# Performance work log

Hardware: AMD Instinct MI355X
Metric: run time of the kernel (lower is better)

## Reference

```python
import jax, jax.numpy as jnp
import numpy as np

NUM_RAYS = 262144   # 512x512 image
NUM_BINS = 128      # coarse samples per ray
NUM_SAMPLES = 128   # fine samples per ray (init arg)
EPS = 1e-05


def setup_inputs() -> dict:
    key = jax.random.key(0)
    k1, k2 = jax.random.split(key)
    weights = jax.random.uniform(k1, (NUM_RAYS, NUM_BINS), dtype=jnp.float32)
    u = jax.random.uniform(k2, (NUM_RAYS, NUM_SAMPLES), dtype=jnp.float32)
    return {"weights": weights, "u": u, "stratified": 1}


def reference(weights, u, stratified):
    # --- pdf normalization (visible torch code) ---
    num_bins = weights.shape[-1]
    num_samples = u.shape[-1]
    weights_sum = jnp.sum(weights, axis=-1, keepdims=True)
    padding = jax.nn.relu(EPS - weights_sum)
    weights = weights + padding / num_bins
    weights_sum = weights_sum + padding
    pdf = weights / weights_sum                                   # [R, B]

    # --- CDF ---
    cdf = jnp.cumsum(pdf, axis=-1)
    cdf = jnp.concatenate([jnp.zeros_like(cdf[..., :1]), cdf], axis=-1)  # [R, B+1]

    # --- stratified / deterministic uniforms in [0,1) ---
    strata = jnp.arange(num_samples, dtype=weights.dtype)
    if stratified:
        us = (strata + u) / num_samples                           # [R, S]
    else:
        us = jnp.broadcast_to((strata + 0.5) / num_samples, u.shape)

    # --- inverse-CDF: searchsorted + gather + lerp ---
    inds = jax.vmap(lambda c, uu: jnp.searchsorted(c, uu, side='right'))(cdf, us)
    below = jnp.clip(inds - 1, 0, num_bins)                       # [R, S]
    above = jnp.clip(inds, 0, num_bins)
    cdf_b = jnp.take_along_axis(cdf, below, axis=-1)
    cdf_a = jnp.take_along_axis(cdf, above, axis=-1)
    bins = jnp.linspace(0.0, 1.0, num_bins + 1, dtype=weights.dtype)  # normalized bin edges
    bins_b = bins[below]
    bins_a = bins[above]
    denom = cdf_a - cdf_b
    denom = jnp.where(denom < 1e-5, jnp.ones_like(denom), denom)
    t = (us - cdf_b) / denom
    samples = bins_b + t * (bins_a - bins_b)                      # [R, S]
    return samples
```

## Files before the change

### kernel.cpp

```cpp
#include <hip/hip_runtime.h>


typedef float f32x4 __attribute__((ext_vector_type(4)));

constexpr int NUM_BINS = 128;
constexpr float EPS_PAD = 1e-5f;
constexpr float INV_S   = 1.0f / 128.0f;
constexpr int RPB       = 8;

template <int CTRL, int ROW_MASK>
__device__ __forceinline__ float dpp_add(float x) {
    int s = __builtin_amdgcn_update_dpp(0, __float_as_int(x), CTRL, ROW_MASK, 0xf, true);
    return x + __int_as_float(s);
}

__global__ __launch_bounds__(256) void ray_sampler_kernel(
    const float* __restrict__ W,
    const float* __restrict__ U,
    const int*   __restrict__ stratp,
    float*       __restrict__ out)
{
    const int wave = threadIdx.x >> 6;
    const int lane = threadIdx.x & 63;
    const int h    = lane >> 5;
    const int sl   = lane & 31;
    const int ray  = blockIdx.x * RPB + wave * 2 + h;

    __shared__ float cdf_s[RPB][NUM_BINS];
    float* cw = cdf_s[wave * 2 + h];

    const size_t rb = (size_t)ray * NUM_BINS;
    const int strat = *stratp;

    const float ur0 = U[rb + sl];
    const float ur1 = U[rb + sl + 32];
    const float ur2 = U[rb + sl + 64];
    const float ur3 = U[rb + sl + 96];

    const int b = 4 * sl;
    const f32x4 w4 = *reinterpret_cast<const f32x4*>(W + rb + b);

    const float s1 = w4.x;
    const float s2 = s1 + w4.y;
    const float s3 = s2 + w4.z;
    const float quad = s3 + w4.w;

    float incl = quad;
    incl = dpp_add<0x111, 0xf>(incl);
    incl = dpp_add<0x112, 0xf>(incl);
    incl = dpp_add<0x114, 0xf>(incl);
    incl = dpp_add<0x118, 0xf>(incl);
    incl = dpp_add<0x142, 0xa>(incl);

    const float tot = __shfl(incl, 31 | (lane & 32), 64);
    const float padding = fmaxf(EPS_PAD - tot, 0.0f);
    const float ppb     = padding * INV_S;
    const float inv     = __builtin_amdgcn_rcpf(tot + padding);
    const float pre     = incl - quad;

    f32x4 st;
    st.x = (pre + s1   + (float)(b + 1) * ppb) * inv;
    st.y = (pre + s2   + (float)(b + 2) * ppb) * inv;
    st.z = (pre + s3   + (float)(b + 3) * ppb) * inv;
    st.w = (pre + quad + (float)(b + 4) * ppb) * inv;
    *reinterpret_cast<f32x4*>(cw + b) = st;

    asm volatile("s_waitcnt lgkmcnt(0)" ::: "memory");

    const float uu0 = strat ? ur0 : 0.5f;
    const float uu1 = strat ? ur1 : 0.5f;
    const float uu2 = strat ? ur2 : 0.5f;
    const float uu3 = strat ? ur3 : 0.5f;
    const float us0 = ((float)(sl)      + uu0) * INV_S;
    const float us1 = ((float)(sl + 32) + uu1) * INV_S;
    const float us2 = ((float)(sl + 64) + uu2) * INV_S;
    const float us3 = ((float)(sl + 96) + uu3) * INV_S;

    int a0 = 0, a1 = 0, a2 = 0, a3 = 0;
    #pragma unroll
    for (int step = 64; step; step >>= 1) {
        const float c0 = cw[a0 + (step - 1)];
        const float c1 = cw[a1 + (step - 1)];
        const float c2 = cw[a2 + (step - 1)];
        const float c3 = cw[a3 + (step - 1)];
        if (c0 <= us0) a0 += step;
        if (c1 <= us1) a1 += step;
        if (c2 <= us2) a2 += step;
        if (c3 <= us3) a3 += step;
    }

    const int m0 = a0 ? a0 - 1 : 0;
    const int m1 = a1 ? a1 - 1 : 0;
    const int m2 = a2 ? a2 - 1 : 0;
    const int m3 = a3 ? a3 - 1 : 0;
    const float lo0 = cw[m0], hi0 = cw[m0 + 1];
    const float lo1 = cw[m1], hi1 = cw[m1 + 1];
    const float lo2 = cw[m2], hi2 = cw[m2 + 1];
    const float lo3 = cw[m3], hi3 = cw[m3 + 1];
    const float cb0 = a0 ? lo0 : 0.0f, ca0 = a0 ? hi0 : lo0;
    const float cb1 = a1 ? lo1 : 0.0f, ca1 = a1 ? hi1 : lo1;
    const float cb2 = a2 ? lo2 : 0.0f, ca2 = a2 ? hi2 : lo2;
    const float cb3 = a3 ? lo3 : 0.0f, ca3 = a3 ? hi3 : lo3;

    float d0 = ca0 - cb0;  d0 = (d0 < 1e-5f) ? 1.0f : d0;
    float d1 = ca1 - cb1;  d1 = (d1 < 1e-5f) ? 1.0f : d1;
    float d2 = ca2 - cb2;  d2 = (d2 < 1e-5f) ? 1.0f : d2;
    float d3 = ca3 - cb3;  d3 = (d3 < 1e-5f) ? 1.0f : d3;

    const float o0 = ((float)a0 + (us0 - cb0) * __builtin_amdgcn_rcpf(d0)) * INV_S;
    const float o1 = ((float)a1 + (us1 - cb1) * __builtin_amdgcn_rcpf(d1)) * INV_S;
    const float o2 = ((float)a2 + (us2 - cb2) * __builtin_amdgcn_rcpf(d2)) * INV_S;
    const float o3 = ((float)a3 + (us3 - cb3) * __builtin_amdgcn_rcpf(d3)) * INV_S;

    __builtin_nontemporal_store(o0, out + rb + sl);
    __builtin_nontemporal_store(o1, out + rb + sl + 32);
    __builtin_nontemporal_store(o2, out + rb + sl + 64);
    __builtin_nontemporal_store(o3, out + rb + sl + 96);
}

extern "C" void kernel_launch(void* const* d_in, const int* in_sizes, int n_in,
                              void* d_out, int out_size, void* d_ws, size_t ws_size,
                              hipStream_t stream) {
    const float* W     = (const float*)d_in[0];
    const float* U     = (const float*)d_in[1];
    const int*   strat = (const int*)d_in[2];
    float*       out   = (float*)d_out;

    const int num_rays = in_sizes[0] / NUM_BINS;
    const int blocks   = num_rays / RPB;
    hipLaunchKernelGGL(ray_sampler_kernel, dim3(blocks), dim3(256), 0, stream,
                       W, U, strat, out);
}
```

Baseline: 60.57 us.

## Resolve top binary-search levels from registers and use bit-reversed LDS layout

The CDF is now stored in LDS in a bit-reversed (Eytzinger-like) order, and the first three binary-search levels take their pivots from readlane'd scalar values instead of LDS. The remaining four levels read LDS at addresses that fit the bit-reversed layout, and the lower/upper CDF bracket is tracked during the search, so the final two gathers go away. The shuffle for the row total is replaced with readlanes. This cuts LDS traffic and dependent LDS latency on the search path, at the cost of scalar readlanes, extra selects, and scalar LDS stores in place of a vector store.

```diff
diff --git a/kernel.cpp b/kernel.cpp
--- a/kernel.cpp
+++ b/kernel.cpp
@@ -12,6 +12,10 @@
 __device__ __forceinline__ float dpp_add(float x) {
     int s = __builtin_amdgcn_update_dpp(0, __float_as_int(x), CTRL, ROW_MASK, 0xf, true);
     return x + __int_as_float(s);
+}
+
+__device__ __forceinline__ float rl(float v, int lane) {
+    return __int_as_float(__builtin_amdgcn_readlane(__float_as_int(v), lane));
 }
 
 __global__ __launch_bounds__(256) void ray_sampler_kernel(
@@ -39,7 +43,6 @@
 
     const int b = 4 * sl;
     const f32x4 w4 = *reinterpret_cast<const f32x4*>(W + rb + b);
-
     const float s1 = w4.x;
     const float s2 = s1 + w4.y;
     const float s3 = s2 + w4.z;
@@ -52,7 +55,8 @@
     incl = dpp_add<0x118, 0xf>(incl);
     incl = dpp_add<0x142, 0xa>(incl);
 
-    const float tot = __shfl(incl, 31 | (lane & 32), 64);
+    const float totA = rl(incl, 31), totB = rl(incl, 63);
+    const float tot  = h ? totB : totA;
     const float padding = fmaxf(EPS_PAD - tot, 0.0f);
     const float ppb     = padding * INV_S;
     const float inv     = __builtin_amdgcn_rcpf(tot + padding);
@@ -63,7 +67,21 @@
     st.y = (pre + s2   + (float)(b + 2) * ppb) * inv;
     st.z = (pre + s3   + (float)(b + 3) * ppb) * inv;
     st.w = (pre + quad + (float)(b + 4) * ppb) * inv;
-    *reinterpret_cast<f32x4*>(cw + b) = st;
+
+    const int r5 = (int)(__brev((unsigned)sl) >> 27);
+    cw[r5]      = st.x;
+    cw[r5 + 64] = st.y;
+    cw[r5 + 32] = st.z;
+    cw[r5 + 96] = st.w;
+
+    const float v16  = h ? rl(st.w, 35) : rl(st.w, 3);
+    const float v32  = h ? rl(st.w, 39) : rl(st.w, 7);
+    const float v48  = h ? rl(st.w, 43) : rl(st.w, 11);
+    const float v64  = h ? rl(st.w, 47) : rl(st.w, 15);
+    const float v80  = h ? rl(st.w, 51) : rl(st.w, 19);
+    const float v96  = h ? rl(st.w, 55) : rl(st.w, 23);
+    const float v112 = h ? rl(st.w, 59) : rl(st.w, 27);
+    const float v128 = h ? rl(st.w, 63) : rl(st.w, 31);
 
     asm volatile("s_waitcnt lgkmcnt(0)" ::: "memory");
 
@@ -76,41 +94,46 @@
     const float us2 = ((float)(sl + 64) + uu2) * INV_S;
     const float us3 = ((float)(sl + 96) + uu3) * INV_S;
 
-    int a0 = 0, a1 = 0, a2 = 0, a3 = 0;
-    #pragma unroll
-    for (int step = 64; step; step >>= 1) {
-        const float c0 = cw[a0 + (step - 1)];
-        const float c1 = cw[a1 + (step - 1)];
-        const float c2 = cw[a2 + (step - 1)];
-        const float c3 = cw[a3 + (step - 1)];
-        if (c0 <= us0) a0 += step;
-        if (c1 <= us1) a1 += step;
-        if (c2 <= us2) a2 += step;
-        if (c3 <= us3) a3 += step;
-    }
+    auto search = [&](float us) -> float {
+        const bool p0 = (v64 <= us);
+        float cb = p0 ? v64 : 0.0f;
+        float ca = p0 ? v128 : v64;
+        int sa = p0 ? 1 : 0;
 
-    const int m0 = a0 ? a0 - 1 : 0;
-    const int m1 = a1 ? a1 - 1 : 0;
-    const int m2 = a2 ? a2 - 1 : 0;
-    const int m3 = a3 ? a3 - 1 : 0;
-    const float lo0 = cw[m0], hi0 = cw[m0 + 1];
-    const float lo1 = cw[m1], hi1 = cw[m1 + 1];
-    const float lo2 = cw[m2], hi2 = cw[m2 + 1];
-    const float lo3 = cw[m3], hi3 = cw[m3 + 1];
-    const float cb0 = a0 ? lo0 : 0.0f, ca0 = a0 ? hi0 : lo0;
-    const float cb1 = a1 ? lo1 : 0.0f, ca1 = a1 ? hi1 : lo1;
-    const float cb2 = a2 ? lo2 : 0.0f, ca2 = a2 ? hi2 : lo2;
-    const float cb3 = a3 ? lo3 : 0.0f, ca3 = a3 ? hi3 : lo3;
+        const float m1 = p0 ? v96 : v32;
+        const bool p1 = (m1 <= us);
+        cb = p1 ? m1 : cb;  ca = p1 ? ca : m1;  sa += p1 ? 2 : 0;
 
-    float d0 = ca0 - cb0;  d0 = (d0 < 1e-5f) ? 1.0f : d0;
-    float d1 = ca1 - cb1;  d1 = (d1 < 1e-5f) ? 1.0f : d1;
-    float d2 = ca2 - cb2;  d2 = (d2 < 1e-5f) ? 1.0f : d2;
-    float d3 = ca3 - cb3;  d3 = (d3 < 1e-5f) ? 1.0f : d3;
+        const float m2h = p0 ? v112 : v48;
+        const float m2l = p0 ? v80  : v16;
+        const float m2  = p1 ? m2h : m2l;
+        const bool p2 = (m2 <= us);
+        cb = p2 ? m2 : cb;  ca = p2 ? ca : m2;  sa += p2 ? 4 : 0;
 
-    const float o0 = ((float)a0 + (us0 - cb0) * __builtin_amdgcn_rcpf(d0)) * INV_S;
-    const float o1 = ((float)a1 + (us1 - cb1) * __builtin_amdgcn_rcpf(d1)) * INV_S;
-    const float o2 = ((float)a2 + (us2 - cb2) * __builtin_amdgcn_rcpf(d2)) * INV_S;
-    const float o3 = ((float)a3 + (us3 - cb3) * __builtin_amdgcn_rcpf(d3)) * INV_S;
+        {   const float v = cw[sa + 112];
+            const bool p = (v <= us);
+            cb = p ? v : cb;  ca = p ? ca : v;  sa += p ? 8 : 0;  }
+        {   const float v = cw[sa + 96];
+            const bool p = (v <= us);
+            cb = p ? v : cb;  ca = p ? ca : v;  sa += p ? 16 : 0; }
+        {   const float v = cw[sa + 64];
+            const bool p = (v <= us);
+            cb = p ? v : cb;  ca = p ? ca : v;  sa += p ? 32 : 0; }
+        {   const float v = cw[sa];
+            const bool p = (v <= us);
+            cb = p ? v : cb;  ca = p ? ca : v;  sa += p ? 64 : 0; }
+
+        const int a = (int)(__brev((unsigned)sa) >> 25);
+        float d = ca - cb;
+        d = (d < 1e-5f) ? 1.0f : d;
+        const float t = (us - cb) * __builtin_amdgcn_rcpf(d);
+        return ((float)a + t) * INV_S;
+    };
+
+    const float o0 = search(us0);
+    const float o1 = search(us1);
+    const float o2 = search(us2);
+    const float o3 = search(us3);
 
     __builtin_nontemporal_store(o0, out + rb + sl);
     __builtin_nontemporal_store(o1, out + rb + sl + 32);
```

Measured after the change: 67.42 us. 11.3% more time.

## Process four ray groups per block with software-prefetched loads of the next group

Applied to the files above, without the earlier changes.

Each block now handles 32 rays in four unrolled iterations instead of 8. The next iteration's weights and uniforms are loaded before the current group's scan and search run, so global load latency overlaps with compute. The block count drops fourfold. The cross-lane total now comes from two readlanes instead of a shuffle. This trades more registers and fewer blocks for latency hiding. The shared CDF buffer is reused across iterations, which relies on each wave touching only its own rows.

```diff
diff --git a/kernel.cpp b/kernel.cpp
--- a/kernel.cpp
+++ b/kernel.cpp
@@ -6,12 +6,18 @@
 constexpr int NUM_BINS = 128;
 constexpr float EPS_PAD = 1e-5f;
 constexpr float INV_S   = 1.0f / 128.0f;
-constexpr int RPB       = 8;
+constexpr int ITERS     = 4;
+constexpr int RPI       = 8;
+constexpr int RPB       = RPI * ITERS;
 
 template <int CTRL, int ROW_MASK>
 __device__ __forceinline__ float dpp_add(float x) {
     int s = __builtin_amdgcn_update_dpp(0, __float_as_int(x), CTRL, ROW_MASK, 0xf, true);
     return x + __int_as_float(s);
+}
+
+__device__ __forceinline__ float rl(float v, int lane) {
+    return __int_as_float(__builtin_amdgcn_readlane(__float_as_int(v), lane));
 }
 
 __global__ __launch_bounds__(256) void ray_sampler_kernel(
@@ -24,98 +30,118 @@
     const int lane = threadIdx.x & 63;
     const int h    = lane >> 5;
     const int sl   = lane & 31;
-    const int ray  = blockIdx.x * RPB + wave * 2 + h;
 
-    __shared__ float cdf_s[RPB][NUM_BINS];
+    __shared__ float cdf_s[RPI][NUM_BINS];
     float* cw = cdf_s[wave * 2 + h];
 
-    const size_t rb = (size_t)ray * NUM_BINS;
     const int strat = *stratp;
+    const int b = 4 * sl;
 
-    const float ur0 = U[rb + sl];
-    const float ur1 = U[rb + sl + 32];
-    const float ur2 = U[rb + sl + 64];
-    const float ur3 = U[rb + sl + 96];
+    size_t rb = ((size_t)blockIdx.x * RPB + wave * 2 + h) * NUM_BINS;
+    constexpr size_t RSTEP = (size_t)RPI * NUM_BINS;
 
-    const int b = 4 * sl;
-    const f32x4 w4 = *reinterpret_cast<const f32x4*>(W + rb + b);
+    f32x4 w4  = *reinterpret_cast<const f32x4*>(W + rb + b);
+    float ur0 = U[rb + sl];
+    float ur1 = U[rb + sl + 32];
+    float ur2 = U[rb + sl + 64];
+    float ur3 = U[rb + sl + 96];
 
-    const float s1 = w4.x;
-    const float s2 = s1 + w4.y;
-    const float s3 = s2 + w4.z;
-    const float quad = s3 + w4.w;
+    #pragma unroll
+    for (int i = 0; i < ITERS; ++i) {
+        f32x4 w4n{};
+        float un0 = 0.f, un1 = 0.f, un2 = 0.f, un3 = 0.f;
+        const size_t rbn = rb + RSTEP;
+        if (i < ITERS - 1) {
+            w4n = *reinterpret_cast<const f32x4*>(W + rbn + b);
+            un0 = U[rbn + sl];
+            un1 = U[rbn + sl + 32];
+            un2 = U[rbn + sl + 64];
+            un3 = U[rbn + sl + 96];
+        }
 
-    float incl = quad;
-    incl = dpp_add<0x111, 0xf>(incl);
-    incl = dpp_add<0x112, 0xf>(incl);
-    incl = dpp_add<0x114, 0xf>(incl);
-    incl = dpp_add<0x118, 0xf>(incl);
-    incl = dpp_add<0x142, 0xa>(incl);
+        const float s1 = w4.x;
+        const float s2 = s1 + w4.y;
+        const float s3 = s2 + w4.z;
+        const float quad = s3 + w4.w;
 
-    const float tot = __shfl(incl, 31 | (lane & 32), 64);
-    const float padding = fmaxf(EPS_PAD - tot, 0.0f);
-    const float ppb     = padding * INV_S;
-    const float inv     = __builtin_amdgcn_rcpf(tot + padding);
-    const float pre     = incl - quad;
+        float incl = quad;
+        incl = dpp_add<0x111, 0xf>(incl);
+        incl = dpp_add<0x112, 0xf>(incl);
+        incl = dpp_add<0x114, 0xf>(incl);
+        incl = dpp_add<0x118, 0xf>(incl);
+        incl = dpp_add<0x142, 0xa>(incl);
 
-    f32x4 st;
-    st.x = (pre + s1   + (float)(b + 1) * ppb) * inv;
-    st.y = (pre + s2   + (float)(b + 2) * ppb) * inv;
-    st.z = (pre + s3   + (float)(b + 3) * ppb) * inv;
-    st.w = (pre + quad + (float)(b + 4) * ppb) * inv;
-    *reinterpret_cast<f32x4*>(cw + b) = st;
+        const float totA = rl(incl, 31), totB = rl(incl, 63);
+        const float tot  = h ? totB : totA;
+        const float padding = fmaxf(EPS_PAD - tot, 0.0f);
+        const float ppb     = padding * INV_S;
+        const float inv     = __builtin_amdgcn_rcpf(tot + padding);
+        const float pre     = incl - quad;
 
-    asm volatile("s_waitcnt lgkmcnt(0)" ::: "memory");
+        f32x4 st;
+        st.x = (pre + s1   + (float)(b + 1) * ppb) * inv;
+        st.y = (pre + s2   + (float)(b + 2) * ppb) * inv;
+        st.z = (pre + s3   + (float)(b + 3) * ppb) * inv;
+        st.w = (pre + quad + (float)(b + 4) * ppb) * inv;
+        *reinterpret_cast<f32x4*>(cw + b) = st;
 
-    const float uu0 = strat ? ur0 : 0.5f;
-    const float uu1 = strat ? ur1 : 0.5f;
-    const float uu2 = strat ? ur2 : 0.5f;
-    const float uu3 = strat ? ur3 : 0.5f;
-    const float us0 = ((float)(sl)      + uu0) * INV_S;
-    const float us1 = ((float)(sl + 32) + uu1) * INV_S;
-    const float us2 = ((float)(sl + 64) + uu2) * INV_S;
-    const float us3 = ((float)(sl + 96) + uu3) * INV_S;
+        asm volatile("s_waitcnt lgkmcnt(0)" ::: "memory");
 
-    int a0 = 0, a1 = 0, a2 = 0, a3 = 0;
-    #pragma unroll
-    for (int step = 64; step; step >>= 1) {
-        const float c0 = cw[a0 + (step - 1)];
-        const float c1 = cw[a1 + (step - 1)];
-        const float c2 = cw[a2 + (step - 1)];
-        const float c3 = cw[a3 + (step - 1)];
-        if (c0 <= us0) a0 += step;
-        if (c1 <= us1) a1 += step;
-        if (c2 <= us2) a2 += step;
-        if (c3 <= us3) a3 += step;
+        const float uu0 = strat ? ur0 : 0.5f;
+        const float uu1 = strat ? ur1 : 0.5f;
+        const float uu2 = strat ? ur2 : 0.5f;
+        const float uu3 = strat ? ur3 : 0.5f;
+        const float us0 = ((float)(sl)      + uu0) * INV_S;
+        const float us1 = ((float)(sl + 32) + uu1) * INV_S;
+        const float us2 = ((float)(sl + 64) + uu2) * INV_S;
+        const float us3 = ((float)(sl + 96) + uu3) * INV_S;
+
+        int a0 = 0, a1 = 0, a2 = 0, a3 = 0;
+        #pragma unroll
+        for (int step = 64; step; step >>= 1) {
+            const float c0 = cw[a0 + (step - 1)];
+            const float c1 = cw[a1 + (step - 1)];
+            const float c2 = cw[a2 + (step - 1)];
+            const float c3 = cw[a3 + (step - 1)];
+            if (c0 <= us0) a0 += step;
+            if (c1 <= us1) a1 += step;
+            if (c2 <= us2) a2 += step;
+            if (c3 <= us3) a3 += step;
+        }
+
+        const int m0 = a0 ? a0 - 1 : 0;
+        const int m1 = a1 ? a1 - 1 : 0;
+        const int m2 = a2 ? a2 - 1 : 0;
+        const int m3 = a3 ? a3 - 1 : 0;
+        const float lo0 = cw[m0], hi0 = cw[m0 + 1];
+        const float lo1 = cw[m1], hi1 = cw[m1 + 1];
+        const float lo2 = cw[m2], hi2 = cw[m2 + 1];
+        const float lo3 = cw[m3], hi3 = cw[m3 + 1];
+        const float cb0 = a0 ? lo0 : 0.0f, ca0 = a0 ? hi0 : lo0;
+        const float cb1 = a1 ? lo1 : 0.0f, ca1 = a1 ? hi1 : lo1;
+        const float cb2 = a2 ? lo2 : 0.0f, ca2 = a2 ? hi2 : lo2;
+        const float cb3 = a3 ? lo3 : 0.0f, ca3 = a3 ? hi3 : lo3;
+
+        float d0 = ca0 - cb0;  d0 = (d0 < 1e-5f) ? 1.0f : d0;
+        float d1 = ca1 - cb1;  d1 = (d1 < 1e-5f) ? 1.0f : d1;
+        float d2 = ca2 - cb2;  d2 = (d2 < 1e-5f) ? 1.0f : d2;
+        float d3 = ca3 - cb3;  d3 = (d3 < 1e-5f) ? 1.0f : d3;
+
+        const float o0 = ((float)a0 + (us0 - cb0) * __builtin_amdgcn_rcpf(d0)) * INV_S;
+        const float o1 = ((float)a1 + (us1 - cb1) * __builtin_amdgcn_rcpf(d1)) * INV_S;
+        const float o2 = ((float)a2 + (us2 - cb2) * __builtin_amdgcn_rcpf(d2)) * INV_S;
+        const float o3 = ((float)a3 + (us3 - cb3) * __builtin_amdgcn_rcpf(d3)) * INV_S;
+
+        __builtin_nontemporal_store(o0, out + rb + sl);
+        __builtin_nontemporal_store(o1, out + rb + sl + 32);
+        __builtin_nontemporal_store(o2, out + rb + sl + 64);
+        __builtin_nontemporal_store(o3, out + rb + sl + 96);
+
+        if (i < ITERS - 1) {
+            w4 = w4n; ur0 = un0; ur1 = un1; ur2 = un2; ur3 = un3;
+            rb = rbn;
+        }
     }
-
-    const int m0 = a0 ? a0 - 1 : 0;
-    const int m1 = a1 ? a1 - 1 : 0;
-    const int m2 = a2 ? a2 - 1 : 0;
-    const int m3 = a3 ? a3 - 1 : 0;
-    const float lo0 = cw[m0], hi0 = cw[m0 + 1];
-    const float lo1 = cw[m1], hi1 = cw[m1 + 1];
-    const float lo2 = cw[m2], hi2 = cw[m2 + 1];
-    const float lo3 = cw[m3], hi3 = cw[m3 + 1];
-    const float cb0 = a0 ? lo0 : 0.0f, ca0 = a0 ? hi0 : lo0;
-    const float cb1 = a1 ? lo1 : 0.0f, ca1 = a1 ? hi1 : lo1;
-    const float cb2 = a2 ? lo2 : 0.0f, ca2 = a2 ? hi2 : lo2;
-    const float cb3 = a3 ? lo3 : 0.0f, ca3 = a3 ? hi3 : lo3;
-
-    float d0 = ca0 - cb0;  d0 = (d0 < 1e-5f) ? 1.0f : d0;
-    float d1 = ca1 - cb1;  d1 = (d1 < 1e-5f) ? 1.0f : d1;
-    float d2 = ca2 - cb2;  d2 = (d2 < 1e-5f) ? 1.0f : d2;
-    float d3 = ca3 - cb3;  d3 = (d3 < 1e-5f) ? 1.0f : d3;
-
-    const float o0 = ((float)a0 + (us0 - cb0) * __builtin_amdgcn_rcpf(d0)) * INV_S;
-    const float o1 = ((float)a1 + (us1 - cb1) * __builtin_amdgcn_rcpf(d1)) * INV_S;
-    const float o2 = ((float)a2 + (us2 - cb2) * __builtin_amdgcn_rcpf(d2)) * INV_S;
-    const float o3 = ((float)a3 + (us3 - cb3) * __builtin_amdgcn_rcpf(d3)) * INV_S;
-
-    __builtin_nontemporal_store(o0, out + rb + sl);
-    __builtin_nontemporal_store(o1, out + rb + sl + 32);
-    __builtin_nontemporal_store(o2, out + rb + sl + 64);
-    __builtin_nontemporal_store(o3, out + rb + sl + 96);
 }
 
 extern "C" void kernel_launch(void* const* d_in, const int* in_sizes, int n_in,
```

After: 65.75 us. 8.6% more time.
